# Performance work log

Measured on AMD Instinct MI355X. Metric: run time of the kernel, lower is better.

The kernel has to match this reference:

```python
import jax, jax.numpy as jnp
import numpy as np

B, F_, E = 4096, 40, 64
T, M, H = 2, 3, 1
EPS = 1e-5


def setup_inputs() -> dict:
    key = jax.random.key(0)
    ks = jax.random.split(key, 8)
    def xavier(k, shape, fan_in, fan_out):
        a = float(np.sqrt(6.0 / (fan_in + fan_out)))
        return jax.random.uniform(k, shape, jnp.float32, -a, a)
    x = jax.random.normal(ks[0], (B, F_, E), jnp.float32)
    masker = xavier(ks[1], (T, M, F_, F_), F_, F_)
    ln_gamma = jnp.ones((F_,), jnp.float32)
    ln_beta = jnp.zeros((F_,), jnp.float32)
    w_t = xavier(ks[2], (1, T, H, 2 * E, E), 2 * E, E)
    b_t = xavier(ks[3], (T, H, F_, E), F_, E)
    nbn = T * F_ * 2 * E
    bn_gamma = jnp.ones((nbn,), jnp.float32)
    bn_beta = jnp.zeros((nbn,), jnp.float32)
    bn_mean = jnp.zeros((nbn,), jnp.float32)
    bn_var = jnp.ones((nbn,), jnp.float32)
    gate_w = xavier(ks[4], (F_ * E, F_), F_ * E, F_)
    gate_b = jnp.zeros((F_,), jnp.float32)
    return {"x": x, "masker": masker, "ln_gamma": ln_gamma, "ln_beta": ln_beta,
            "w_t": w_t, "b_t": b_t, "bn_gamma": bn_gamma, "bn_beta": bn_beta,
            "bn_mean": bn_mean, "bn_var": bn_var, "gate_w": gate_w, "gate_b": gate_b}


def reference(x, masker, ln_gamma, ln_beta, w_t, b_t, bn_gamma, bn_beta, bn_mean, bn_var, gate_w, gate_b):
    b = x.shape[0]
    # broadcast input across towers: (B, T, F, E)
    xt = jnp.broadcast_to(x[:, None], (b, T, F_, E))
    # masked adjacency construction (per tower)
    adj = jax.nn.relu(jnp.prod(masker, axis=1))            # (T, F, F)
    mask = (adj != 0).astype(x.dtype)
    # LayerNorm over dim -2 (applied to transposed adj in torch)
    t = jnp.swapaxes(adj, -1, -2)
    mu = t.mean(-1, keepdims=True)
    var = t.var(-1, keepdims=True)
    t = (t - mu) / jnp.sqrt(var + EPS) * ln_gamma + ln_beta
    adj = jnp.swapaxes(t, -1, -2)
    logits = adj + (1.0 - mask) * (-1e9) + jnp.eye(F_, dtype=x.dtype)
    adj = jax.nn.softmax(logits, axis=1) * mask            # softmax over source-field dim
    xcur = xt
    for idx in range(H):
        # neighbor aggregation: nei[b,t,f,e] = sum_g x[b,t,g,e] * adj[t,g,f]
        nei = jnp.einsum('btge,tgf->btfe', xcur, adj)
        xc = jnp.concatenate([xcur, nei], axis=-1)         # (B, T, F, 2E)
        flat = xc.reshape(b, -1)                           # BatchNorm1d, inference mode
        flat = (flat - bn_mean) / jnp.sqrt(bn_var + EPS) * bn_gamma + bn_beta
        xc = flat.reshape(b, T, F_, 2 * E)
        xcur = jnp.einsum('btfk,tke->btfe', xc, w_t[0, :, idx]) + b_t[:, idx]
    # gating over fields
    g = xcur.reshape(b, T, F_ * E) @ gate_w + gate_b       # (B, T, F)
    w = jax.nn.softmax(g, axis=2)
    return jnp.sum(xcur * w[..., None], axis=2)            # (B, T, E)
```

## Files before the change

### kernel.cpp

```cpp
#include <hip/hip_runtime.h>
#include <hip/hip_bf16.h>
#include <math.h>

#define Fdim 40
#define Edim 64
#define Tdim 2
#define EPSV 1e-5f

typedef __attribute__((ext_vector_type(8))) short short8;
typedef __attribute__((ext_vector_type(4))) float f32x4;

__device__ __forceinline__ short f2b(float f) {
    unsigned u = __builtin_bit_cast(unsigned, f);
    unsigned r = (u + 0x7fffu + ((u >> 16) & 1u)) >> 16;
    return (short)r;
}
__device__ __forceinline__ float b2f(short h) {
    unsigned u = ((unsigned)(unsigned short)h) << 16;
    return __builtin_bit_cast(float, u);
}
__device__ __forceinline__ f32x4 mfma16(short8 a, short8 b, f32x4 c) {
    return __builtin_amdgcn_mfma_f32_16x16x32_bf16(a, b, c, 0, 0, 0);
}
__device__ __forceinline__ int swz(int f, int e2 ) {
    return (f * 128 + e2) ^ ((f & 7) << 4);
}

#define BUFS 5152


__global__ void adj_kernel(const float* __restrict__ masker,
                           const float* __restrict__ ln_gamma,
                           const float* __restrict__ ln_beta,
                           short* __restrict__ adjF) {
    const int t = blockIdx.x;
    const int tid = threadIdx.x;
    __shared__ float araw[Fdim][Fdim];

    for (int i = tid; i < Fdim * Fdim; i += 64) {
        int g = i / Fdim, ff = i % Fdim;
        const float* mb = masker + t * (3 * Fdim * Fdim) + g * Fdim + ff;
        float p = mb[0] * mb[Fdim * Fdim] * mb[2 * Fdim * Fdim];
        araw[g][ff] = p > 0.f ? p : 0.f;
    }
    __syncthreads();

    const int f = tid;
    float vals[Fdim];
    if (f < 40) {
        float mu = 0.f, m2 = 0.f;
        #pragma unroll
        for (int g = 0; g < Fdim; ++g) {
            float v = araw[g][f];
            mu += v; m2 += v * v;
        }
        mu *= (1.f / Fdim); m2 *= (1.f / Fdim);
        float inv = rsqrtf(m2 - mu * mu + EPSV);

        float mx = -1e30f;
        #pragma unroll
        for (int g = 0; g < Fdim; ++g) {
            float v = araw[g][f];
            float l = (v - mu) * inv * ln_gamma[g] + ln_beta[g];
            if (v == 0.f) l += -1e9f;
            if (g == f) l += 1.f;
            vals[g] = l;
            mx = fmaxf(mx, l);
        }
        float den = 0.f;
        #pragma unroll
        for (int g = 0; g < Fdim; ++g) {
            float p = expf(vals[g] - mx);
            vals[g] = p;
            den += p;
        }
        float rden = 1.f / den;
        #pragma unroll
        for (int g = 0; g < Fdim; ++g) {
            float msk = (araw[g][f] != 0.f) ? 1.f : 0.f;
            vals[g] = vals[g] * rden * msk;
        }
    }
    if (f < 48) {
        int er = f & 15, mt = f >> 4;
        short8* dst = (short8*)adjF;
        #pragma unroll
        for (int kt = 0; kt < 2; ++kt) {
            #pragma unroll
            for (int qq = 0; qq < 4; ++qq) {
                short8 v;
                #pragma unroll
                for (int j = 0; j < 8; ++j) {
                    int g = kt * 32 + qq * 8 + j;
                    v[j] = (f < 40 && g < 40) ? f2b(vals[g]) : (short)0;
                }
                dst[((t * 3 + mt) * 2 + kt) * 64 + qq * 16 + er] = v;
            }
        }
    }
}

__global__ void prep_kernel(const float* __restrict__ w_t,
                            const float* __restrict__ gate_w,
                            const float* __restrict__ bn_gamma,
                            const float* __restrict__ bn_beta,
                            const float* __restrict__ bn_mean,
                            const float* __restrict__ bn_var,
                            const float* __restrict__ b_t,
                            short* __restrict__ WF,
                            short* __restrict__ gwF,
                            float* __restrict__ bnSxF,
                            float* __restrict__ bnOxF,
                            float* __restrict__ bn2SF,
                            float* __restrict__ bn2OF,
                            float* __restrict__ btF) {
    int i = blockIdx.x * 256 + threadIdx.x;
    if (i < 16384) {
        int j = i & 7, l = (i >> 3) & 63, nt = (i >> 9) & 3, kt = (i >> 11) & 3, t = i >> 13;
        int k = kt * 32 + (l >> 4) * 8 + j, e = nt * 16 + (l & 15);
        WF[i] = f2b(w_t[t * 8192 + k * 64 + e]);
    } else if (i < 139264) {
        int idx = i - 16384;
        int j = idx & 7, l = (idx >> 3) & 63, r = idx >> 9;
        int nt = r % 3, kk = r / 3;
        int fo = nt * 16 + (l & 15), k = kk * 32 + (l >> 4) * 8 + j;
        gwF[idx] = (fo < 40) ? f2b(gate_w[(size_t)k * 40 + fo]) : (short)0;
    } else if (i < 145408) {
        int idx = i - 139264;
        int c = idx & 3, l = (idx >> 2) & 63, h = (idx >> 8) & 1, kt = (idx >> 9) & 1, tm = idx >> 10;
        int mt = tm % 3, t = tm / 3;
        int f = mt * 16 + (l & 15), k = kt * 32 + (l >> 4) * 8 + h * 4 + c;
        float sv = 0.f, ov = 0.f;
        if (f < 40) {
            int src = t * 5120 + f * 128 + k;
            sv = bn_gamma[src] * rsqrtf(bn_var[src] + EPSV);
            ov = bn_beta[src] - bn_mean[src] * sv;
        }
        bnSxF[idx] = sv; bnOxF[idx] = ov;
    } else if (i < 151552) {
        int idx = i - 145408;
        int rr = idx & 3, l = (idx >> 2) & 63, nt = (idx >> 8) & 3, tm = idx >> 10;
        int mt = tm % 3, t = tm / 3;
        int f = mt * 16 + (l >> 4) * 4 + rr, e = nt * 16 + (l & 15);
        float sv = 0.f, ov = 0.f;
        if (f < 40) {
            int src = t * 5120 + f * 128 + 64 + e;
            sv = bn_gamma[src] * rsqrtf(bn_var[src] + EPSV);
            ov = bn_beta[src] - bn_mean[src] * sv;
        }
        bn2SF[idx] = sv; bn2OF[idx] = ov;
    } else if (i < 157696) {
        int idx = i - 151552;
        int rr = idx & 3, l = (idx >> 2) & 63, nt = (idx >> 8) & 3, tm = idx >> 10;
        int mt = tm % 3, t = tm / 3;
        int f = mt * 16 + (l >> 4) * 4 + rr, e = nt * 16 + (l & 15);
        btF[idx] = (f < 40) ? b_t[t * 2560 + f * 64 + e] : 0.f;
    }
}

__global__ __launch_bounds__(256, 4) void main_kernel(
    const float* __restrict__ x,
    const short* __restrict__ adjF,
    const short* __restrict__ WF,
    const short* __restrict__ gwF,
    const f32x4* __restrict__ bnSxF,
    const f32x4* __restrict__ bnOxF,
    const f32x4* __restrict__ bn2SF,
    const f32x4* __restrict__ bn2OF,
    const f32x4* __restrict__ btF,
    const float* __restrict__ gate_b,
    float* __restrict__ out)
{
    extern __shared__ char smem[];
    const int tid = threadIdx.x;
    const int w = tid >> 6, lane = tid & 63;
    const int er = lane & 15, q = lane >> 4;
    const int s = w >> 1, t = w & 1;
    const int bbase = blockIdx.x * 2;

    char* buf = smem + w * BUFS;
    f32x4* gred = (f32x4*)(smem + 4 * BUFS);
    float* g_lds = (float*)(smem + 4 * BUFS + 3072);

    const float* xb = x + (size_t)(bbase + s) * 2560;
    const short8* adjF8 = (const short8*)adjF;
    const short8* WF8   = (const short8*)WF;
    const short8* gwF8  = (const short8*)gwF;

    short8 Bf[2][4];
    #pragma unroll
    for (int nt = 0; nt < 4; ++nt) {
        const float* xe = xb + nt * 16 + er;
        short8 v0;
        #pragma unroll
        for (int j = 0; j < 8; ++j) v0[j] = f2b(xe[(q * 8 + j) * 64]);
        Bf[0][nt] = v0;
        short8 v1 = {0, 0, 0, 0, 0, 0, 0, 0};
        if (q == 0) {
            #pragma unroll
            for (int j = 0; j < 8; ++j) v1[j] = f2b(xe[(32 + j) * 64]);
        }
        Bf[1][nt] = v1;
    }

    #pragma unroll
    for (int mt = 0; mt < 3; ++mt) {
        short8 A0 = adjF8[((t * 3 + mt) * 2 + 0) * 64 + lane];
        short8 A1 = adjF8[((t * 3 + mt) * 2 + 1) * 64 + lane];
        #pragma unroll
        for (int nt = 0; nt < 4; ++nt) {
            f32x4 z = {0.f, 0.f, 0.f, 0.f};
            z = mfma16(A0, Bf[0][nt], z);
            f32x4 acc = mfma16(A1, Bf[1][nt], z);
            f32x4 s2 = bn2SF[((t * 3 + mt) * 4 + nt) * 64 + lane];
            f32x4 o2 = bn2OF[((t * 3 + mt) * 4 + nt) * 64 + lane];
            int e = nt * 16 + er;
            #pragma unroll
            for (int r = 0; r < 4; ++r) {
                int f = mt * 16 + q * 4 + r;
                if (f < 40) {
                    float vv = acc[r] * s2[r] + o2[r];
                    *(short*)(buf + swz(f, e * 2)) = f2b(vv);
                }
            }
        }
    }

    #pragma unroll
    for (int mt = 0; mt < 3; ++mt) {
        f32x4 acc[4];
        #pragma unroll
        for (int nt = 0; nt < 4; ++nt) { f32x4 z = {0.f,0.f,0.f,0.f}; acc[nt] = z; }
        #pragma unroll
        for (int kt = 0; kt < 4; ++kt) {
            short8 A;
            if (kt < 2) {
                int f = mt * 16 + er;
                if (f < 40) {
                    const float4* xp = (const float4*)(xb + f * 64 + kt * 32 + q * 8);
                    float4 x0 = xp[0], x1 = xp[1];
                    int fb = (((t * 3 + mt) * 2 + kt) * 2) * 64 + lane;
                    f32x4 s0 = bnSxF[fb], s1 = bnSxF[fb + 64];
                    f32x4 o0 = bnOxF[fb], o1 = bnOxF[fb + 64];
                    A[0] = f2b(x0.x * s0[0] + o0[0]);
                    A[1] = f2b(x0.y * s0[1] + o0[1]);
                    A[2] = f2b(x0.z * s0[2] + o0[2]);
                    A[3] = f2b(x0.w * s0[3] + o0[3]);
                    A[4] = f2b(x1.x * s1[0] + o1[0]);
                    A[5] = f2b(x1.y * s1[1] + o1[1]);
                    A[6] = f2b(x1.z * s1[2] + o1[2]);
                    A[7] = f2b(x1.w * s1[3] + o1[3]);
                } else {
                    short8 za = {0,0,0,0,0,0,0,0};
                    A = za;
                }
            } else {
                int f = mt * 16 + er;
                int fr = (f < 40) ? f : (f - 8);
                A = *(const short8*)(buf + swz(fr, (kt - 2) * 64 + q * 16));
            }
            #pragma unroll
            for (int nt = 0; nt < 4; ++nt) {
                short8 B = WF8[((t * 4 + kt) * 4 + nt) * 64 + lane];
                acc[nt] = mfma16(A, B, acc[nt]);
            }
        }
        #pragma unroll
        for (int nt = 0; nt < 4; ++nt) {
            f32x4 bt4 = btF[((t * 3 + mt) * 4 + nt) * 64 + lane];
            int e = nt * 16 + er;
            #pragma unroll
            for (int r = 0; r < 4; ++r) {
                int f = mt * 16 + q * 4 + r;
                if (f < 40) {
                    float vv = acc[nt][r] + bt4[r];
                    *(short*)(buf + swz(f, e * 2)) = f2b(vv);
                }
            }
        }
    }

    __syncthreads();

    f32x4 g0 = {0.f,0.f,0.f,0.f}, g1 = g0, g2 = g0;
    {
        const char* abase = smem + (er & 3) * BUFS;
        #pragma unroll
        for (int kk = 0; kk < 20; ++kk) {
            int step = w * 20 + kk;
            int k0 = step * 32;
            int f = k0 >> 6;
            short8 A = *(const short8*)(abase + swz(f, (k0 & 63) * 2 + q * 16));
            const short8* gp = gwF8 + (size_t)step * 3 * 64 + lane;
            g0 = mfma16(A, gp[0], g0);
            g1 = mfma16(A, gp[64], g1);
            g2 = mfma16(A, gp[128], g2);
        }
    }
    if (w < 2 && q < 2) {
        gred[(w * 3 + 0) * 32 + (lane & 31)] = g0;
        gred[(w * 3 + 1) * 32 + (lane & 31)] = g1;
        gred[(w * 3 + 2) * 32 + (lane & 31)] = g2;
    }
    __syncthreads();
    if (w >= 2 && q < 2) {
        gred[((w - 2) * 3 + 0) * 32 + (lane & 31)] += g0;
        gred[((w - 2) * 3 + 1) * 32 + (lane & 31)] += g1;
        gred[((w - 2) * 3 + 2) * 32 + (lane & 31)] += g2;
    }
    __syncthreads();

    if (tid < 192) {
        int nt = tid >> 6, l = tid & 63;
        if (l < 16) {
            f32x4 v = gred[(0 * 3 + nt) * 32 + l] + gred[(1 * 3 + nt) * 32 + l];
            int fo = nt * 16 + l;
            if (fo < 40) {
                float gb = gate_b[fo];
                #pragma unroll
                for (int r = 0; r < 4; ++r)
                    g_lds[r * 40 + fo] = v[r] + gb;
            }
        }
    }
    __syncthreads();

    {
        int st = tid >> 6, e = tid & 63;
        const float* gr = g_lds + st * 40;
        const char* bufr = smem + st * BUFS;
        float m = gr[0];
        #pragma unroll
        for (int f2 = 1; f2 < 40; ++f2) m = fmaxf(m, gr[f2]);
        float den = 0.f, o = 0.f;
        #pragma unroll
        for (int f2 = 0; f2 < 40; ++f2) {
            float p = __expf(gr[f2] - m);
            den += p;
            short xv = *(const short*)(bufr + swz(f2, e * 2));
            o += p * b2f(xv);
        }
        out[(size_t)(blockIdx.x * 4 + st) * 64 + e] = o / den;
    }
}

extern "C" void kernel_launch(void* const* d_in, const int* in_sizes, int n_in,
                              void* d_out, int out_size, void* d_ws, size_t ws_size,
                              hipStream_t stream) {
    (void)in_sizes; (void)n_in; (void)out_size; (void)ws_size;
    const float* x        = (const float*)d_in[0];
    const float* masker   = (const float*)d_in[1];
    const float* ln_gamma = (const float*)d_in[2];
    const float* ln_beta  = (const float*)d_in[3];
    const float* w_t      = (const float*)d_in[4];
    const float* b_t      = (const float*)d_in[5];
    const float* bn_gamma = (const float*)d_in[6];
    const float* bn_beta  = (const float*)d_in[7];
    const float* bn_mean  = (const float*)d_in[8];
    const float* bn_var   = (const float*)d_in[9];
    const float* gate_w   = (const float*)d_in[10];
    const float* gate_b   = (const float*)d_in[11];
    float* out = (float*)d_out;

    short* adjFp  = (short*)d_ws;
    short* WFp    = adjFp + 6144;
    short* gwFp   = WFp + 16384;
    float* bnSxFp = (float*)(gwFp + 122880);
    float* bnOxFp = bnSxFp + 6144;
    float* bn2SFp = bnOxFp + 6144;
    float* bn2OFp = bn2SFp + 6144;
    float* btFp   = bn2OFp + 6144;

    adj_kernel<<<Tdim, 64, 0, stream>>>(masker, ln_gamma, ln_beta, adjFp);
    prep_kernel<<<616, 256, 0, stream>>>(w_t, gate_w, bn_gamma, bn_beta, bn_mean,
                                         bn_var, b_t, WFp, gwFp, bnSxFp, bnOxFp,
                                         bn2SFp, bn2OFp, btFp);

    constexpr int SMEM_BYTES = 4 * BUFS + 3072 + 640;
    main_kernel<<<2048, 256, SMEM_BYTES, stream>>>(
        x, adjFp, (const short*)WFp, (const short*)gwFp,
        (const f32x4*)bnSxFp, (const f32x4*)bnOxFp,
        (const f32x4*)bn2SFp, (const f32x4*)bn2OFp,
        (const f32x4*)btFp, gate_b, out);
}
```

Baseline: 78.32 us.

## Process both towers per wave, four samples per block

Each wave now handles one batch sample for both towers instead of one (sample, tower) pair, so each block covers four samples and the grid is halved. The x tile is loaded and converted to bf16 once and feeds both towers' neighbor aggregation and transform MFMAs. The gate GEMM and the softmax pooling are widened to eight sample-tower rows. The cost is more registers per wave (two accumulator sets) and twice the LDS per block, which may lower occupancy.

```diff
diff --git a/kernel.cpp b/kernel.cpp
--- a/kernel.cpp
+++ b/kernel.cpp
@@ -175,14 +175,14 @@
     const int tid = threadIdx.x;
     const int w = tid >> 6, lane = tid & 63;
     const int er = lane & 15, q = lane >> 4;
-    const int s = w >> 1, t = w & 1;
-    const int bbase = blockIdx.x * 2;
-
-    char* buf = smem + w * BUFS;
-    f32x4* gred = (f32x4*)(smem + 4 * BUFS);
-    float* g_lds = (float*)(smem + 4 * BUFS + 3072);
-
-    const float* xb = x + (size_t)(bbase + s) * 2560;
+    const int bbase = blockIdx.x * 4;
+
+    char* buf0 = smem + (w * 2 + 0) * BUFS;
+    char* buf1 = smem + (w * 2 + 1) * BUFS;
+    f32x4* gred = (f32x4*)(smem + 8 * BUFS);
+    float* g_lds = (float*)(smem + 8 * BUFS + 3072);
+
+    const float* xb = x + (size_t)(bbase + w) * 2560;
     const short8* adjF8 = (const short8*)adjF;
     const short8* WF8   = (const short8*)WF;
     const short8* gwF8  = (const short8*)gwF;
@@ -205,22 +205,26 @@
 
     #pragma unroll
     for (int mt = 0; mt < 3; ++mt) {
-        short8 A0 = adjF8[((t * 3 + mt) * 2 + 0) * 64 + lane];
-        short8 A1 = adjF8[((t * 3 + mt) * 2 + 1) * 64 + lane];
+        short8 A00 = adjF8[((0 * 3 + mt) * 2 + 0) * 64 + lane];
+        short8 A01 = adjF8[((0 * 3 + mt) * 2 + 1) * 64 + lane];
+        short8 A10 = adjF8[((1 * 3 + mt) * 2 + 0) * 64 + lane];
+        short8 A11 = adjF8[((1 * 3 + mt) * 2 + 1) * 64 + lane];
         #pragma unroll
         for (int nt = 0; nt < 4; ++nt) {
             f32x4 z = {0.f, 0.f, 0.f, 0.f};
-            z = mfma16(A0, Bf[0][nt], z);
-            f32x4 acc = mfma16(A1, Bf[1][nt], z);
-            f32x4 s2 = bn2SF[((t * 3 + mt) * 4 + nt) * 64 + lane];
-            f32x4 o2 = bn2OF[((t * 3 + mt) * 4 + nt) * 64 + lane];
+            f32x4 a0 = mfma16(A01, Bf[1][nt], mfma16(A00, Bf[0][nt], z));
+            f32x4 a1 = mfma16(A11, Bf[1][nt], mfma16(A10, Bf[0][nt], z));
+            f32x4 s20 = bn2SF[((0 * 3 + mt) * 4 + nt) * 64 + lane];
+            f32x4 o20 = bn2OF[((0 * 3 + mt) * 4 + nt) * 64 + lane];
+            f32x4 s21 = bn2SF[((1 * 3 + mt) * 4 + nt) * 64 + lane];
+            f32x4 o21 = bn2OF[((1 * 3 + mt) * 4 + nt) * 64 + lane];
             int e = nt * 16 + er;
             #pragma unroll
             for (int r = 0; r < 4; ++r) {
                 int f = mt * 16 + q * 4 + r;
                 if (f < 40) {
-                    float vv = acc[r] * s2[r] + o2[r];
-                    *(short*)(buf + swz(f, e * 2)) = f2b(vv);
+                    *(short*)(buf0 + swz(f, e * 2)) = f2b(a0[r] * s20[r] + o20[r]);
+                    *(short*)(buf1 + swz(f, e * 2)) = f2b(a1[r] * s21[r] + o21[r]);
                 }
             }
         }
@@ -228,53 +232,69 @@
 
     #pragma unroll
     for (int mt = 0; mt < 3; ++mt) {
-        f32x4 acc[4];
-        #pragma unroll
-        for (int nt = 0; nt < 4; ++nt) { f32x4 z = {0.f,0.f,0.f,0.f}; acc[nt] = z; }
+        f32x4 acc0[4], acc1[4];
+        #pragma unroll
+        for (int nt = 0; nt < 4; ++nt) {
+            f32x4 z = {0.f,0.f,0.f,0.f};
+            acc0[nt] = z; acc1[nt] = z;
+        }
         #pragma unroll
         for (int kt = 0; kt < 4; ++kt) {
-            short8 A;
+            short8 A0, A1;
             if (kt < 2) {
                 int f = mt * 16 + er;
                 if (f < 40) {
                     const float4* xp = (const float4*)(xb + f * 64 + kt * 32 + q * 8);
                     float4 x0 = xp[0], x1 = xp[1];
-                    int fb = (((t * 3 + mt) * 2 + kt) * 2) * 64 + lane;
-                    f32x4 s0 = bnSxF[fb], s1 = bnSxF[fb + 64];
-                    f32x4 o0 = bnOxF[fb], o1 = bnOxF[fb + 64];
-                    A[0] = f2b(x0.x * s0[0] + o0[0]);
-                    A[1] = f2b(x0.y * s0[1] + o0[1]);
-                    A[2] = f2b(x0.z * s0[2] + o0[2]);
-                    A[3] = f2b(x0.w * s0[3] + o0[3]);
-                    A[4] = f2b(x1.x * s1[0] + o1[0]);
-                    A[5] = f2b(x1.y * s1[1] + o1[1]);
-                    A[6] = f2b(x1.z * s1[2] + o1[2]);
-                    A[7] = f2b(x1.w * s1[3] + o1[3]);
+                    int fb0 = (((0 * 3 + mt) * 2 + kt) * 2) * 64 + lane;
+                    int fb1 = (((1 * 3 + mt) * 2 + kt) * 2) * 64 + lane;
+                    f32x4 s0 = bnSxF[fb0], s1 = bnSxF[fb0 + 64];
+                    f32x4 o0 = bnOxF[fb0], o1 = bnOxF[fb0 + 64];
+                    f32x4 t0 = bnSxF[fb1], t1 = bnSxF[fb1 + 64];
+                    f32x4 p0 = bnOxF[fb1], p1 = bnOxF[fb1 + 64];
+                    A0[0] = f2b(x0.x * s0[0] + o0[0]);
+                    A0[1] = f2b(x0.y * s0[1] + o0[1]);
+                    A0[2] = f2b(x0.z * s0[2] + o0[2]);
+                    A0[3] = f2b(x0.w * s0[3] + o0[3]);
+                    A0[4] = f2b(x1.x * s1[0] + o1[0]);
+                    A0[5] = f2b(x1.y * s1[1] + o1[1]);
+                    A0[6] = f2b(x1.z * s1[2] + o1[2]);
+                    A0[7] = f2b(x1.w * s1[3] + o1[3]);
+                    A1[0] = f2b(x0.x * t0[0] + p0[0]);
+                    A1[1] = f2b(x0.y * t0[1] + p0[1]);
+                    A1[2] = f2b(x0.z * t0[2] + p0[2]);
+                    A1[3] = f2b(x0.w * t0[3] + p0[3]);
+                    A1[4] = f2b(x1.x * t1[0] + p1[0]);
+                    A1[5] = f2b(x1.y * t1[1] + p1[1]);
+                    A1[6] = f2b(x1.z * t1[2] + p1[2]);
+                    A1[7] = f2b(x1.w * t1[3] + p1[3]);
                 } else {
                     short8 za = {0,0,0,0,0,0,0,0};
-                    A = za;
+                    A0 = za; A1 = za;
                 }
             } else {
                 int f = mt * 16 + er;
                 int fr = (f < 40) ? f : (f - 8);
-                A = *(const short8*)(buf + swz(fr, (kt - 2) * 64 + q * 16));
+                A0 = *(const short8*)(buf0 + swz(fr, (kt - 2) * 64 + q * 16));
+                A1 = *(const short8*)(buf1 + swz(fr, (kt - 2) * 64 + q * 16));
             }
             #pragma unroll
             for (int nt = 0; nt < 4; ++nt) {
-                short8 B = WF8[((t * 4 + kt) * 4 + nt) * 64 + lane];
-                acc[nt] = mfma16(A, B, acc[nt]);
+                acc0[nt] = mfma16(A0, WF8[((0 * 4 + kt) * 4 + nt) * 64 + lane], acc0[nt]);
+                acc1[nt] = mfma16(A1, WF8[((1 * 4 + kt) * 4 + nt) * 64 + lane], acc1[nt]);
             }
         }
         #pragma unroll
         for (int nt = 0; nt < 4; ++nt) {
-            f32x4 bt4 = btF[((t * 3 + mt) * 4 + nt) * 64 + lane];
+            f32x4 b0 = btF[((0 * 3 + mt) * 4 + nt) * 64 + lane];
+            f32x4 b1 = btF[((1 * 3 + mt) * 4 + nt) * 64 + lane];
             int e = nt * 16 + er;
             #pragma unroll
             for (int r = 0; r < 4; ++r) {
                 int f = mt * 16 + q * 4 + r;
                 if (f < 40) {
-                    float vv = acc[nt][r] + bt4[r];
-                    *(short*)(buf + swz(f, e * 2)) = f2b(vv);
+                    *(short*)(buf0 + swz(f, e * 2)) = f2b(acc0[nt][r] + b0[r]);
+                    *(short*)(buf1 + swz(f, e * 2)) = f2b(acc1[nt][r] + b1[r]);
                 }
             }
         }
@@ -284,7 +304,7 @@
 
     f32x4 g0 = {0.f,0.f,0.f,0.f}, g1 = g0, g2 = g0;
     {
-        const char* abase = smem + (er & 3) * BUFS;
+        const char* abase = smem + (er & 7) * BUFS;
         #pragma unroll
         for (int kk = 0; kk < 20; ++kk) {
             int step = w * 20 + kk;
@@ -312,35 +332,40 @@
 
     if (tid < 192) {
         int nt = tid >> 6, l = tid & 63;
-        if (l < 16) {
+        if (l < 32) {
+            int rer = l & 15, rq = l >> 4;
             f32x4 v = gred[(0 * 3 + nt) * 32 + l] + gred[(1 * 3 + nt) * 32 + l];
-            int fo = nt * 16 + l;
+            int fo = nt * 16 + rer;
             if (fo < 40) {
                 float gb = gate_b[fo];
                 #pragma unroll
                 for (int r = 0; r < 4; ++r)
-                    g_lds[r * 40 + fo] = v[r] + gb;
+                    g_lds[(rq * 4 + r) * 40 + fo] = v[r] + gb;
             }
         }
     }
     __syncthreads();
 
     {
-        int st = tid >> 6, e = tid & 63;
-        const float* gr = g_lds + st * 40;
-        const char* bufr = smem + st * BUFS;
-        float m = gr[0];
-        #pragma unroll
-        for (int f2 = 1; f2 < 40; ++f2) m = fmaxf(m, gr[f2]);
-        float den = 0.f, o = 0.f;
-        #pragma unroll
-        for (int f2 = 0; f2 < 40; ++f2) {
-            float p = __expf(gr[f2] - m);
-            den += p;
-            short xv = *(const short*)(bufr + swz(f2, e * 2));
-            o += p * b2f(xv);
-        }
-        out[(size_t)(blockIdx.x * 4 + st) * 64 + e] = o / den;
+        int e = tid & 63;
+        #pragma unroll
+        for (int rep = 0; rep < 2; ++rep) {
+            int st = (tid >> 6) + rep * 4;
+            const float* gr = g_lds + st * 40;
+            const char* bufr = smem + st * BUFS;
+            float m = gr[0];
+            #pragma unroll
+            for (int f2 = 1; f2 < 40; ++f2) m = fmaxf(m, gr[f2]);
+            float den = 0.f, o = 0.f;
+            #pragma unroll
+            for (int f2 = 0; f2 < 40; ++f2) {
+                float p = __expf(gr[f2] - m);
+                den += p;
+                short xv = *(const short*)(bufr + swz(f2, e * 2));
+                o += p * b2f(xv);
+            }
+            out[(size_t)(blockIdx.x * 8 + st) * 64 + e] = o / den;
+        }
     }
 }
 
@@ -376,8 +401,8 @@
                                          bn_var, b_t, WFp, gwFp, bnSxFp, bnOxFp,
                                          bn2SFp, bn2OFp, btFp);
 
-    constexpr int SMEM_BYTES = 4 * BUFS + 3072 + 640;
-    main_kernel<<<2048, 256, SMEM_BYTES, stream>>>(
+    constexpr int SMEM_BYTES = 8 * BUFS + 3072 + 1280;
+    main_kernel<<<1024, 256, SMEM_BYTES, stream>>>(
         x, adjFp, (const short*)WFp, (const short*)gwFp,
         (const f32x4*)bnSxFp, (const f32x4*)bnOxFp,
         (const f32x4*)bn2SFp, (const f32x4*)bn2OFp,
```

Result: slower. 133.4 us (+70.3%).
